# Optimization experiments

Hardware: AMD Instinct MI355X
Metric: run time of the kernel (lower is better)

The kernel has to match this reference:

```python
import jax, jax.numpy as jnp
import numpy as np
from jax import lax

B, W, S, D, H, BH, C = 32, 128, 192, 768, 10, 30, 50
NEG = -1e30  # stand-in for -inf to keep grads NaN-free


def _lstm_dir(x, Wih, Whh, bih, bhh, reverse):
    # x: [B, T, D] -> [B, T, H]; torch gate order i, f, g, o
    xg = jnp.einsum('btd,gd->btg', x, Wih) + bih  # [B, T, 4H]
    if reverse:
        xg = xg[:, ::-1]

    def step(carry, g_t):
        h, c = carry
        g = g_t + h @ Whh.T + bhh
        i, f, gg, o = jnp.split(g, 4, axis=-1)
        c = jax.nn.sigmoid(f) * c + jax.nn.sigmoid(i) * jnp.tanh(gg)
        h = jax.nn.sigmoid(o) * jnp.tanh(c)
        return (h, c), h

    init = (jnp.zeros((x.shape[0], H), x.dtype), jnp.zeros((x.shape[0], H), x.dtype))
    _, hs = lax.scan(step, init, xg.transpose(1, 0, 2))
    hs = hs.transpose(1, 0, 2)
    if reverse:
        hs = hs[:, ::-1]
    return hs


def _biaffine(x, W1, b1, W2, b2, U, bias):
    # DeepBiaffineScorer: MLP+ReLU on each side, bilinear with bias-augmented inputs
    h1 = jax.nn.relu(x @ W1 + b1)
    h2 = jax.nn.relu(x @ W2 + b2)
    ones = jnp.ones(h1.shape[:-1] + (1,), h1.dtype)
    h1a = jnp.concatenate([h1, ones], -1)  # [B, W, BH+1]
    h2a = jnp.concatenate([h2, ones], -1)
    return jnp.einsum('bih,ohg,bjg->bijo', h1a, U, h2a) + bias  # [B, W, W, O]


def _ce_sum(logits, targets, ignore):
    # cross-entropy, reduction='sum', with ignore_index; classes on last axis
    logp = jax.nn.log_softmax(logits, -1)
    valid = targets != ignore
    t = jnp.where(valid, targets, 0)
    picked = jnp.take_along_axis(logp, t[..., None], -1).squeeze(-1)
    return -jnp.sum(jnp.where(valid, picked, 0.0))


def _forward(hiddens, bert2toks, heads, dep_rels, masks,
             Wih_f, Whh_f, bih_f, bhh_f, Wih_b, Whh_b, bih_b, bhh_b,
             un_W1, un_b1, un_W2, un_b2, un_U, un_bias,
             dr_W1, dr_b1, dr_W2, dr_b2, dr_U, dr_bias):
    # mean of the 3 selected BERT layers, then ragged subtoken -> word mean pooling
    means = jnp.mean(hiddens, axis=0)  # [B, S+1, D]
    sub = means[:, 1:]                 # skip [CLS]: [B, S, D]
    seg_sum = jax.vmap(lambda x, s: jax.ops.segment_sum(x, s, num_segments=W))(sub, bert2toks)
    cnt = jax.vmap(lambda s: jax.ops.segment_sum(jnp.ones((S,), sub.dtype), s, num_segments=W))(bert2toks)
    bert_out = seg_sum / jnp.maximum(cnt, 1.0)[..., None]  # [B, W, D]

    # BiLSTM (sent_lens are all full length W, so packing is the identity)
    fwd = _lstm_dir(bert_out, Wih_f, Whh_f, bih_f, bhh_f, False)
    bwd = _lstm_dir(bert_out, Wih_b, Whh_b, bih_b, bhh_b, True)
    unpacked = jnp.concatenate([fwd, bwd], -1)  # [B, W, 2H]

    unlabeled = _biaffine(unpacked, un_W1, un_b1, un_W2, un_b2, un_U, un_bias)[..., 0]  # [B, W, W]
    deprel = _biaffine(unpacked, dr_W1, dr_b1, dr_W2, dr_b2, dr_U, dr_bias)             # [B, W, W, C]

    eye = jnp.eye(W, dtype=bool)
    unlabeled = jnp.where(eye[None], NEG, unlabeled)

    # gather gold-head deprel scores: [B, W, C]
    head_scores = jnp.take_along_axis(deprel, heads[:, :, None, None], axis=2).squeeze(2)
    heads_ = jnp.where(masks, -1, heads)

    deprel_loss = _ce_sum(head_scores, dep_rels, 0)
    depind_loss = _ce_sum(unlabeled[:, 1:], heads_[:, 1:], -1)
    return deprel_loss + depind_loss


def setup_inputs() -> dict:
    key = jax.random.key(0)
    ks = jax.random.split(key, 26)
    hiddens = jax.random.normal(ks[0], (3, B, S + 1, D), jnp.float32)
    # non-decreasing subtoken->word map covering all W words
    bert2toks = jnp.broadcast_to((jnp.arange(S) * W) // S, (B, S)).astype(jnp.int32)
    heads = jax.random.randint(ks[1], (B, W), 0, W)
    heads = jnp.where(heads == jnp.arange(W)[None, :], 0, heads)  # no self-head (diag is -inf)
    dep_rels = jax.random.randint(ks[2], (B, W), 0, C)
    masks = jnp.zeros((B, W), bool)
    sent_lens = jnp.full((B,), W, jnp.int32)
    s = 0.1
    p = lambda k, shape: jax.random.normal(k, shape, jnp.float32) * s
    return dict(
        hiddens=hiddens, bert2toks=bert2toks, heads=heads, dep_rels=dep_rels,
        masks=masks, sent_lens=sent_lens,
        Wih_f=p(ks[3], (4 * H, D)), Whh_f=p(ks[4], (4 * H, H)), bih_f=p(ks[5], (4 * H,)), bhh_f=p(ks[6], (4 * H,)),
        Wih_b=p(ks[7], (4 * H, D)), Whh_b=p(ks[8], (4 * H, H)), bih_b=p(ks[9], (4 * H,)), bhh_b=p(ks[10], (4 * H,)),
        un_W1=p(ks[11], (2 * H, BH)), un_b1=p(ks[12], (BH,)), un_W2=p(ks[13], (2 * H, BH)), un_b2=p(ks[14], (BH,)),
        un_U=p(ks[15], (1, BH + 1, BH + 1)), un_bias=p(ks[16], (1,)),
        dr_W1=p(ks[17], (2 * H, BH)), dr_b1=p(ks[18], (BH,)), dr_W2=p(ks[19], (2 * H, BH)), dr_b2=p(ks[20], (BH,)),
        dr_U=p(ks[21], (C, BH + 1, BH + 1)), dr_bias=p(ks[22], (C,)),
    )


def reference(hiddens, bert2toks, heads, dep_rels, masks, sent_lens,
              Wih_f, Whh_f, bih_f, bhh_f, Wih_b, Whh_b, bih_b, bhh_b,
              un_W1, un_b1, un_W2, un_b2, un_U, un_bias,
              dr_W1, dr_b1, dr_W2, dr_b2, dr_U, dr_bias):
    # sent_lens unused: all sentences are full length, so pack/unpack is identity
    return _forward(hiddens, bert2toks, heads, dep_rels, masks,
                    Wih_f, Whh_f, bih_f, bhh_f, Wih_b, Whh_b, bih_b, bhh_b,
                    un_W1, un_b1, un_W2, un_b2, un_U, un_bias,
                    dr_W1, dr_b1, dr_W2, dr_b2, dr_U, dr_bias)
```

## Files before the change

kernel.cpp:

```cpp
#include <hip/hip_runtime.h>

#define Bn 32
#define Wn 128
#define Sn 192
#define Dn 768
#define Hn 10
#define BHn 30
#define Cn 50
#define NEGV -1e30f

typedef _Float16 h2 __attribute__((ext_vector_type(2)));
typedef _Float16 h8 __attribute__((ext_vector_type(8)));
typedef __fp16 fp16x2 __attribute__((ext_vector_type(2)));
union H8u { h8 v; h2 p[4]; float4 f; };

__device__ __forceinline__ float fsig(float x) {
    return __builtin_amdgcn_rcpf(1.0f + __expf(-x));
}
__device__ __forceinline__ float ftanh(float x) {
    return 1.0f - 2.0f * __builtin_amdgcn_rcpf(1.0f + __expf(2.0f * x));
}
__device__ __forceinline__ float lane_bcast(float v, int srclane) {
    union { float f; int i; } u, w;
    u.f = v;
    w.i = __builtin_amdgcn_readlane(u.i, srclane);
    return w.f;
}
template <int Q>
__device__ __forceinline__ float quad_bcast(float v) {
    union { float f; int i; } u, w;
    u.f = v;
    w.i = __builtin_amdgcn_mov_dpp(u.i, (Q << 6) | (Q << 4) | (Q << 2) | Q, 0xf, 0xf, true);
    return w.f;
}
__device__ __forceinline__ h2 pk16(float a, float b) {
#if __has_builtin(__builtin_amdgcn_cvt_pkrtz)
    union { fp16x2 r; h2 h; } u;
    u.r = __builtin_amdgcn_cvt_pkrtz(a, b);
    return u.h;
#else
    h2 r; r[0] = (_Float16)a; r[1] = (_Float16)b; return r;
#endif
}
__device__ __forceinline__ float dot2f(h2 a, h2 b, float c) {
#if __has_builtin(__builtin_amdgcn_fdot2)
    return __builtin_amdgcn_fdot2(a, b, c, false);
#else
    return c + (float)a[0] * (float)b[0] + (float)a[1] * (float)b[1];
#endif
}

#define XSTR2 52
__global__ __launch_bounds__(256) void k_tokproj(const float* __restrict__ hid,
                                                 const float* __restrict__ Wf,
                                                 const float* __restrict__ Wb,
                                                 float* __restrict__ tokg4,
                                                 float* __restrict__ out) {
    __shared__ h2 xl[64 * XSTR2];
    __shared__ h2 wl[80 * XSTR2];
    int tb = blockIdx.x >> 3;
    int kq = blockIdx.x & 7;
    int b = tb / 3;
    int s0 = (tb % 3) * 64;
    int k0 = kq * 96;
    int tid = threadIdx.x;
    if (blockIdx.x == 0 && tid == 0) out[0] = 0.f;

    for (int idx = tid; idx < 64 * 24; idx += 256) {
        int r = idx / 24, k4 = idx % 24;
        size_t rowbase = ((size_t)b * (Sn + 1) + (s0 + r + 1)) * Dn + k0 + 4 * k4;
        float4 v0 = *(const float4*)(hid + rowbase);
        float4 v1 = *(const float4*)(hid + (size_t)Bn * (Sn + 1) * Dn + rowbase);
        float4 v2 = *(const float4*)(hid + (size_t)2 * Bn * (Sn + 1) * Dn + rowbase);
        h2 a = pk16(v0.x + v1.x + v2.x, v0.y + v1.y + v2.y);
        h2 bb = pk16(v0.z + v1.z + v2.z, v0.w + v1.w + v2.w);
        xl[r * XSTR2 + 2 * k4] = a;
        xl[r * XSTR2 + 2 * k4 + 1] = bb;
    }
    for (int idx = tid; idx < 80 * 24; idx += 256) {
        int co = idx / 24, k4 = idx % 24;
        int dir = co / 40, off = co % 40;
        int j = off >> 2, g = off & 3;
        const float4 w = *(const float4*)((dir ? Wb : Wf) + (g * 10 + j) * Dn + k0 + 4 * k4);
        wl[co * XSTR2 + 2 * k4] = pk16(w.x, w.y);
        wl[co * XSTR2 + 2 * k4 + 1] = pk16(w.z, w.w);
    }
    __syncthreads();

    int tg = tid >> 4;
    int rg = tid & 15;
    float acc[4][5];
#pragma unroll
    for (int tt = 0; tt < 4; ++tt)
#pragma unroll
        for (int rr = 0; rr < 5; ++rr) acc[tt][rr] = 0.f;

    for (int kk = 0; kk < 12; ++kk) {
        H8u xv[4], wv[5];
#pragma unroll
        for (int tt = 0; tt < 4; ++tt)
            xv[tt].v = *(const h8*)(xl + (tg * 4 + tt) * XSTR2 + kk * 4);
#pragma unroll
        for (int rr = 0; rr < 5; ++rr)
            wv[rr].v = *(const h8*)(wl + (rg * 5 + rr) * XSTR2 + kk * 4);
#pragma unroll
        for (int tt = 0; tt < 4; ++tt)
#pragma unroll
            for (int rr = 0; rr < 5; ++rr) {
                float a = acc[tt][rr];
                a = dot2f(xv[tt].p[0], wv[rr].p[0], a);
                a = dot2f(xv[tt].p[1], wv[rr].p[1], a);
                a = dot2f(xv[tt].p[2], wv[rr].p[2], a);
                a = dot2f(xv[tt].p[3], wv[rr].p[3], a);
                acc[tt][rr] = a;
            }
    }
    size_t nbase = (size_t)kq * (Bn * Sn) + (size_t)b * Sn + s0;
#pragma unroll
    for (int tt = 0; tt < 4; ++tt) {
        size_t ob = (nbase + tg * 4 + tt) * 80 + rg * 5;
#pragma unroll
        for (int rr = 0; rr < 5; ++rr) tokg4[ob + rr] = acc[tt][rr];
    }
}

__global__ __launch_bounds__(96) void k_wordmean(const float* __restrict__ tokg4,
                                                 const int* __restrict__ b2t,
                                                 const float* __restrict__ bih_f,
                                                 const float* __restrict__ bih_b,
                                                 float* __restrict__ xg) {
    const size_t NT80 = (size_t)Bn * Sn * 80;
    int bw = blockIdx.x;
    int b = bw >> 7, w = bw & 127;
    int tid = threadIdx.x;
    __shared__ int ws[Sn];
    ws[tid] = b2t[b * Sn + tid];
    ws[96 + tid] = b2t[b * Sn + 96 + tid];
    __syncthreads();
    if (tid >= 80) return;
    int dir = tid / 40, off = tid % 40;
    float acc = 0.f;
    int cnt = 0;
    for (int s = 0; s < Sn; ++s) {
        if (ws[s] == w) {
            ++cnt;
            size_t base = ((size_t)b * Sn + s) * 80 + tid;
#pragma unroll
            for (int p = 0; p < 8; ++p) acc += tokg4[base + p * NT80];
        }
    }
    float inv = 1.0f / (3.0f * (float)(cnt > 0 ? cnt : 1));
    int brow = (off & 3) * 10 + (off >> 2);
    float bias = (dir ? bih_b : bih_f)[brow];
    xg[((size_t)(dir * Bn + b) * Wn + w) * 40 + off] = acc * inv + bias;
}

__global__ __launch_bounds__(64) void k_lstm(const float* __restrict__ xg,
                                             const float* __restrict__ Whh_f, const float* __restrict__ bhh_f,
                                             const float* __restrict__ Whh_b, const float* __restrict__ bhh_b,
                                             float* __restrict__ hs) {
    int lane = threadIdx.x;
    int seq = blockIdx.x;
    int dir = seq >> 5;
    int l = lane < 40 ? lane : 39;
    int j = l >> 2, G = l & 3;

    const float* Whh = dir ? Whh_b : Whh_f;
    const float* bhh = dir ? bhh_b : bhh_f;
    float wk[Hn];
#pragma unroll
    for (int k = 0; k < Hn; ++k) wk[k] = Whh[(G * Hn + j) * Hn + k];
    float bias = bhh[G * Hn + j];

    const float* xbase = xg + (size_t)seq * Wn * 40;
    float* hbase = hs + (size_t)seq * Wn * Hn;
    bool st = (G == 0) && (lane < 40);

    float h = 0.f, c = 0.f;
    int dt = dir ? -1 : 1;
    int t = dir ? (Wn - 1) : 0;
    float xq[8];
#pragma unroll
    for (int q = 0; q < 7; ++q) xq[q] = xbase[(t + q * dt) * 40 + l];

#pragma unroll 8
    for (int step = 0; step < Wn; ++step) {
        float xv = xq[step & 7];
        xq[(step + 7) & 7] = xbase[(t + 7 * dt) * 40 + l];
        float hb[Hn];
#pragma unroll
        for (int k = 0; k < Hn; ++k) hb[k] = lane_bcast(h, 4 * k);
        float ga = xv, gb = bias;
#pragma unroll
        for (int k = 0; k < 5; ++k) ga += wk[k] * hb[k];
#pragma unroll
        for (int k = 5; k < Hn; ++k) gb += wk[k] * hb[k];
        float g = ga + gb;
        float gin = (G == 2) ? 2.f * g : g;
        float s = fsig(gin);
        float av = (G == 2) ? 2.f * s - 1.f : s;
        float ai = quad_bcast<0>(av);
        float af = quad_bcast<1>(av);
        float ag = quad_bcast<2>(av);
        float ao = quad_bcast<3>(av);
        c = af * c + ai * ag;
        h = ao * ftanh(c);
        if (st) hbase[t * Hn + j] = h;
        t += dt;
    }
}

__global__ __launch_bounds__(128) void k_mlp(const float* __restrict__ hs,
                                             const float* __restrict__ uW1, const float* __restrict__ ub1,
                                             const float* __restrict__ uW2, const float* __restrict__ ub2,
                                             const float* __restrict__ dW1, const float* __restrict__ db1,
                                             const float* __restrict__ dW2, const float* __restrict__ db2,
                                             float* __restrict__ hpad) {
    int bt = blockIdx.x;
    int b = bt / Wn, t = bt % Wn;
    __shared__ float x[20];
    int tid = threadIdx.x;
    if (tid < 20) {
        x[tid] = (tid < Hn) ? hs[((size_t)(0 * Bn + b) * Wn + t) * Hn + tid]
                            : hs[((size_t)(1 * Bn + b) * Wn + t) * Hn + (tid - Hn)];
    }
    __syncthreads();
    if (tid >= 124) {
        hpad[((size_t)(tid - 124) * Bn * Wn + bt) * 32 + 31] = 0.f;
        return;
    }
    int which = tid / 31, k = tid % 31;
    float v;
    if (k == 30) {
        v = 1.0f;
    } else {
        const float* Wm;
        const float* bv;
        if (which == 0) { Wm = uW1; bv = ub1; }
        else if (which == 1) { Wm = uW2; bv = ub2; }
        else if (which == 2) { Wm = dW1; bv = db1; }
        else { Wm = dW2; bv = db2; }
        float a = bv[k];
#pragma unroll
        for (int d = 0; d < 20; ++d) a += x[d] * Wm[d * BHn + k];
        v = a > 0.f ? a : 0.f;
    }
    hpad[((size_t)which * Bn * Wn + bt) * 32 + k] = v;
}

__global__ __launch_bounds__(256) void k_drscore(const float* __restrict__ hpad,
                                                 const int* __restrict__ heads,
                                                 const float* __restrict__ U, const float* __restrict__ dbias,
                                                 float* __restrict__ sc) {
    int nc = blockIdx.x & 63;
    int oq = blockIdx.x >> 6;
    __shared__ float Ul[4][992];
    int tid = threadIdx.x;
    for (int idx = tid; idx < 4 * 992; idx += 256) {
        int o = idx / 992, r = idx - o * 992;
        int h = r >> 5, g = r & 31;
        int oo = oq * 4 + o; if (oo >= Cn) oo = Cn - 1;
        Ul[o][r] = (g < 31) ? U[(size_t)oo * 961 + h * 31 + g] : 0.f;
    }
    int w = tid >> 6, lane = tid & 63;
    int o = oq * 4 + w;
    int n = nc * 64 + lane;
    int b = n >> 7;
    int jh = heads[n];
    if (jh < 0 || jh >= Wn) jh = 0;
    const float* h1a = hpad + ((size_t)2 * Bn * Wn + n) * 32;
    const float* h2a = hpad + ((size_t)3 * Bn * Wn + b * Wn + jh) * 32;
    float h2r[32];
    {
        const float4* p = (const float4*)h2a;
#pragma unroll
        for (int q = 0; q < 8; ++q) {
            float4 v = p[q];
            h2r[4 * q + 0] = v.x; h2r[4 * q + 1] = v.y;
            h2r[4 * q + 2] = v.z; h2r[4 * q + 3] = v.w;
        }
    }
    float h1r[32];
    {
        const float4* p = (const float4*)h1a;
#pragma unroll
        for (int q = 0; q < 8; ++q) {
            float4 v = p[q];
            h1r[4 * q + 0] = v.x; h1r[4 * q + 1] = v.y;
            h1r[4 * q + 2] = v.z; h1r[4 * q + 3] = v.w;
        }
    }
    __syncthreads();
    const float* up = Ul[w];
    float acc = 0.f;
    for (int h = 0; h < 31; ++h) {
        float t = 0.f;
#pragma unroll
        for (int g = 0; g < 32; ++g) t += up[h * 32 + g] * h2r[g];
        acc += h1r[h] * t;
    }
    if (o < Cn) sc[(size_t)n * Cn + o] = acc + dbias[o];
}

__global__ __launch_bounds__(256) void k_loss2(const float* __restrict__ hpad,
                                               const float* __restrict__ U0, const float* __restrict__ ubias,
                                               const float* __restrict__ sc,
                                               const int* __restrict__ heads,
                                               const unsigned char* __restrict__ masks,
                                               const int* __restrict__ dep_rels,
                                               float* __restrict__ out) {
    int b = blockIdx.x >> 2;
    int ic = blockIdx.x & 3;
    int tid = threadIdx.x;
    __shared__ float h2s[128 * 36];
    __shared__ float tg[32 * 36];
    __shared__ float U0l[992];
    __shared__ float red[256];
    const float* h1a = hpad + (size_t)b * Wn * 32;
    const float* h2a = hpad + ((size_t)Bn * Wn + b * Wn) * 32;
    for (int idx = tid; idx < 128 * 32; idx += 256)
        h2s[(idx >> 5) * 36 + (idx & 31)] = h2a[idx];
    for (int idx = tid; idx < 992; idx += 256) {
        int g = idx & 31;
        U0l[idx] = (g < 31) ? U0[(idx >> 5) * 31 + g] : 0.f;
    }
    __syncthreads();
    {
        int l = tid & 31, ig = tid >> 5;
        float ur[31];
#pragma unroll
        for (int h = 0; h < 31; ++h) ur[h] = U0l[h * 32 + l];
        for (int ii = 0; ii < 4; ++ii) {
            int il = ig * 4 + ii;
            int i = ic * 32 + il;
            const float4* hp = (const float4*)(h1a + (size_t)i * 32);
            float hr[32];
#pragma unroll
            for (int q = 0; q < 8; ++q) {
                float4 v = hp[q];
                hr[4 * q] = v.x; hr[4 * q + 1] = v.y; hr[4 * q + 2] = v.z; hr[4 * q + 3] = v.w;
            }
            float a = 0.f;
#pragma unroll
            for (int h = 0; h < 31; ++h) a += hr[h] * ur[h];
            tg[il * 36 + l] = a;
        }
    }
    __syncthreads();
    float acc = 0.f;
    {
        int jg = tid & 7, il = tid >> 3;
        int i = ic * 32 + il;
        float ub = ubias[0];
        float4 tq[8];
        const float4* tp = (const float4*)(tg + il * 36);
#pragma unroll
        for (int q = 0; q < 8; ++q) tq[q] = tp[q];
        float m = -3e38f, lsum = 0.f, sh = 0.f;
        int hd = heads[b * Wn + i];
        for (int jj = 0; jj < 16; ++jj) {
            int j = jg * 16 + ((jj + jg) & 15);
            const float4* h2p = (const float4*)(h2s + j * 36);
            float s = ub;
#pragma unroll
            for (int q = 0; q < 8; ++q) {
                float4 hq = h2p[q];
                s += tq[q].x * hq.x + tq[q].y * hq.y + tq[q].z * hq.z + tq[q].w * hq.w;
            }
            if (j == i) s = NEGV;
            float mn = fmaxf(m, s);
            lsum = lsum * __expf(m - mn) + __expf(s - mn);
            m = mn;
            if (j == hd) sh = s;
        }
        float shv = (jg == (hd >> 4)) ? sh : 0.f;
        float mm = m, ll = lsum;
#pragma unroll
        for (int off = 1; off < 8; off <<= 1) {
            float m2 = __shfl_xor(mm, off);
            float l2 = __shfl_xor(ll, off);
            float mn = fmaxf(mm, m2);
            ll = ll * __expf(mm - mn) + l2 * __expf(m2 - mn);
            mm = mn;
            shv += __shfl_xor(shv, off);
        }
        if (jg == 0 && i >= 1 && !masks[b * Wn + i])
            acc += -(shv - (mm + __logf(ll)));
    }
    if (tid < 32) {
        int n = b * Wn + ic * 32 + tid;
        int r = dep_rels[n];
        if (r != 0 && r < Cn) {
            const float* sp = sc + (size_t)n * Cn;
            float mm = sp[0];
            for (int o = 1; o < Cn; ++o) mm = fmaxf(mm, sp[o]);
            float e = 0.f;
            for (int o = 0; o < Cn; ++o) e += __expf(sp[o] - mm);
            acc += -(sp[r] - (mm + __logf(e)));
        }
    }
    red[tid] = acc;
    __syncthreads();
    for (int off = 128; off > 0; off >>= 1) {
        if (tid < off) red[tid] += red[tid + off];
        __syncthreads();
    }
    if (tid == 0) atomicAdd(out, red[0]);
}

extern "C" void kernel_launch(void* const* d_in, const int* in_sizes, int n_in,
                              void* d_out, int out_size, void* d_ws, size_t ws_size,
                              hipStream_t stream) {
    const float* hiddens = (const float*)d_in[0];
    const int* b2t = (const int*)d_in[1];
    const int* heads = (const int*)d_in[2];
    const int* dep_rels = (const int*)d_in[3];
    const unsigned char* masks = (const unsigned char*)d_in[4];
    const float* Wih_f = (const float*)d_in[6];
    const float* Whh_f = (const float*)d_in[7];
    const float* bih_f = (const float*)d_in[8];
    const float* bhh_f = (const float*)d_in[9];
    const float* Wih_b = (const float*)d_in[10];
    const float* Whh_b = (const float*)d_in[11];
    const float* bih_b = (const float*)d_in[12];
    const float* bhh_b = (const float*)d_in[13];
    const float* un_W1 = (const float*)d_in[14];
    const float* un_b1 = (const float*)d_in[15];
    const float* un_W2 = (const float*)d_in[16];
    const float* un_b2 = (const float*)d_in[17];
    const float* un_U  = (const float*)d_in[18];
    const float* un_bias = (const float*)d_in[19];
    const float* dr_W1 = (const float*)d_in[20];
    const float* dr_b1 = (const float*)d_in[21];
    const float* dr_W2 = (const float*)d_in[22];
    const float* dr_b2 = (const float*)d_in[23];
    const float* dr_U  = (const float*)d_in[24];
    const float* dr_bias = (const float*)d_in[25];

    char* p = (char*)d_ws;
    float* tokg4 = (float*)p;     p += (size_t)8 * Bn * Sn * 80 * 4;
    float* xg = (float*)p;        p += (size_t)2 * Bn * Wn * 40 * 4;
    float* hs = (float*)p;        p += (size_t)2 * Bn * Wn * Hn * 4;
    float* hpad = (float*)p;      p += (size_t)4 * Bn * Wn * 32 * 4;
    float* sc = (float*)p;        p += (size_t)Bn * Wn * Cn * 4;

    float* out = (float*)d_out;

    k_tokproj<<<96 * 8, 256, 0, stream>>>(hiddens, Wih_f, Wih_b, tokg4, out);
    k_wordmean<<<Bn * Wn, 96, 0, stream>>>(tokg4, b2t, bih_f, bih_b, xg);
    k_lstm<<<64, 64, 0, stream>>>(xg, Whh_f, bhh_f, Whh_b, bhh_b, hs);
    k_mlp<<<Bn * Wn, 128, 0, stream>>>(hs, un_W1, un_b1, un_W2, un_b2,
                                       dr_W1, dr_b1, dr_W2, dr_b2, hpad);
    k_drscore<<<13 * 64, 256, 0, stream>>>(hpad, heads, dr_U, dr_bias, sc);
    k_loss2<<<Bn * 4, 256, 0, stream>>>(hpad, un_U, un_bias, sc, heads, masks, dep_rels, out);
}
```

Measured before the change: 94.72 us.

## Cut token-projection split-K from 8 to 2 with register-prefetched weight chunks

The token projection kernel now splits the 768-wide reduction into 2 halves instead of 8. Each block loads a 384-wide slice of activations into LDS and walks four weight chunks, prefetching the next chunk into registers while computing the current one. This shrinks the partial-sum buffer by 4x and reduces the word-mean kernel's per-token reads from 8 partials to 2. The cost is only 192 blocks instead of 768, which lowers parallelism, plus more LDS per block and more weight registers, which may reduce occupancy.

Result: slower. 97.05 us (+2.5%).

```diff
diff --git a/kernel.cpp b/kernel.cpp
--- a/kernel.cpp
+++ b/kernel.cpp
@@ -50,40 +50,51 @@
 #endif
 }
 
-#define XSTR2 52
+#define XST 196
+#define WST 52
 __global__ __launch_bounds__(256) void k_tokproj(const float* __restrict__ hid,
                                                  const float* __restrict__ Wf,
                                                  const float* __restrict__ Wb,
-                                                 float* __restrict__ tokg4,
+                                                 float* __restrict__ tokg2,
                                                  float* __restrict__ out) {
-    __shared__ h2 xl[64 * XSTR2];
-    __shared__ h2 wl[80 * XSTR2];
-    int tb = blockIdx.x >> 3;
-    int kq = blockIdx.x & 7;
+    __shared__ h2 xl[64 * XST];
+    __shared__ h2 wl[80 * WST];
+    int tb = blockIdx.x >> 1;
+    int kh = blockIdx.x & 1;
     int b = tb / 3;
     int s0 = (tb % 3) * 64;
-    int k0 = kq * 96;
+    int k0 = kh * 384;
     int tid = threadIdx.x;
     if (blockIdx.x == 0 && tid == 0) out[0] = 0.f;
 
-    for (int idx = tid; idx < 64 * 24; idx += 256) {
-        int r = idx / 24, k4 = idx % 24;
+    float4 wreg[8];
+#define W_ISSUE(kc_) { _Pragma("unroll") \
+    for (int it = 0; it < 8; ++it) { \
+        int idx = tid + it * 256; int ii = idx < 1920 ? idx : 0; \
+        int co = ii / 24, k4 = ii % 24; \
+        int dir = co / 40, off = co % 40; \
+        int jj = off >> 2, gg = off & 3; \
+        wreg[it] = *(const float4*)((dir ? Wb : Wf) + (gg * 10 + jj) * Dn + k0 + (kc_) * 96 + 4 * k4); \
+    } }
+#define W_WRITE() { _Pragma("unroll") \
+    for (int it = 0; it < 8; ++it) { \
+        int idx = tid + it * 256; \
+        if (idx < 1920) { \
+            int co = idx / 24, k4 = idx % 24; \
+            wl[co * WST + 2 * k4] = pk16(wreg[it].x, wreg[it].y); \
+            wl[co * WST + 2 * k4 + 1] = pk16(wreg[it].z, wreg[it].w); \
+        } \
+    } }
+
+    W_ISSUE(0);
+    for (int idx = tid; idx < 64 * 96; idx += 256) {
+        int r = idx / 96, k4 = idx % 96;
         size_t rowbase = ((size_t)b * (Sn + 1) + (s0 + r + 1)) * Dn + k0 + 4 * k4;
         float4 v0 = *(const float4*)(hid + rowbase);
         float4 v1 = *(const float4*)(hid + (size_t)Bn * (Sn + 1) * Dn + rowbase);
         float4 v2 = *(const float4*)(hid + (size_t)2 * Bn * (Sn + 1) * Dn + rowbase);
-        h2 a = pk16(v0.x + v1.x + v2.x, v0.y + v1.y + v2.y);
-        h2 bb = pk16(v0.z + v1.z + v2.z, v0.w + v1.w + v2.w);
-        xl[r * XSTR2 + 2 * k4] = a;
-        xl[r * XSTR2 + 2 * k4 + 1] = bb;
-    }
-    for (int idx = tid; idx < 80 * 24; idx += 256) {
-        int co = idx / 24, k4 = idx % 24;
-        int dir = co / 40, off = co % 40;
-        int j = off >> 2, g = off & 3;
-        const float4 w = *(const float4*)((dir ? Wb : Wf) + (g * 10 + j) * Dn + k0 + 4 * k4);
-        wl[co * XSTR2 + 2 * k4] = pk16(w.x, w.y);
-        wl[co * XSTR2 + 2 * k4 + 1] = pk16(w.z, w.w);
+        xl[r * XST + 2 * k4] = pk16(v0.x + v1.x + v2.x, v0.y + v1.y + v2.y);
+        xl[r * XST + 2 * k4 + 1] = pk16(v0.z + v1.z + v2.z, v0.w + v1.w + v2.w);
     }
     __syncthreads();
 
@@ -95,36 +106,45 @@
 #pragma unroll
         for (int rr = 0; rr < 5; ++rr) acc[tt][rr] = 0.f;
 
-    for (int kk = 0; kk < 12; ++kk) {
-        H8u xv[4], wv[5];
-#pragma unroll
-        for (int tt = 0; tt < 4; ++tt)
-            xv[tt].v = *(const h8*)(xl + (tg * 4 + tt) * XSTR2 + kk * 4);
-#pragma unroll
-        for (int rr = 0; rr < 5; ++rr)
-            wv[rr].v = *(const h8*)(wl + (rg * 5 + rr) * XSTR2 + kk * 4);
-#pragma unroll
-        for (int tt = 0; tt < 4; ++tt)
-#pragma unroll
-            for (int rr = 0; rr < 5; ++rr) {
-                float a = acc[tt][rr];
-                a = dot2f(xv[tt].p[0], wv[rr].p[0], a);
-                a = dot2f(xv[tt].p[1], wv[rr].p[1], a);
-                a = dot2f(xv[tt].p[2], wv[rr].p[2], a);
-                a = dot2f(xv[tt].p[3], wv[rr].p[3], a);
-                acc[tt][rr] = a;
-            }
-    }
-    size_t nbase = (size_t)kq * (Bn * Sn) + (size_t)b * Sn + s0;
+    for (int kc = 0; kc < 4; ++kc) {
+        W_WRITE();
+        __syncthreads();
+        if (kc < 3) W_ISSUE(kc + 1);
+#pragma unroll 2
+        for (int kk = 0; kk < 12; ++kk) {
+            H8u xv[4], wv[5];
+#pragma unroll
+            for (int tt = 0; tt < 4; ++tt)
+                xv[tt].v = *(const h8*)(xl + (tg * 4 + tt) * XST + kc * 48 + kk * 4);
+#pragma unroll
+            for (int rr = 0; rr < 5; ++rr)
+                wv[rr].v = *(const h8*)(wl + (rg * 5 + rr) * WST + kk * 4);
+#pragma unroll
+            for (int tt = 0; tt < 4; ++tt)
+#pragma unroll
+                for (int rr = 0; rr < 5; ++rr) {
+                    float a = acc[tt][rr];
+                    a = dot2f(xv[tt].p[0], wv[rr].p[0], a);
+                    a = dot2f(xv[tt].p[1], wv[rr].p[1], a);
+                    a = dot2f(xv[tt].p[2], wv[rr].p[2], a);
+                    a = dot2f(xv[tt].p[3], wv[rr].p[3], a);
+                    acc[tt][rr] = a;
+                }
+        }
+        __syncthreads();
+    }
+    size_t nbase = (size_t)kh * (Bn * Sn) + (size_t)b * Sn + s0;
 #pragma unroll
     for (int tt = 0; tt < 4; ++tt) {
         size_t ob = (nbase + tg * 4 + tt) * 80 + rg * 5;
 #pragma unroll
-        for (int rr = 0; rr < 5; ++rr) tokg4[ob + rr] = acc[tt][rr];
-    }
-}
-
-__global__ __launch_bounds__(96) void k_wordmean(const float* __restrict__ tokg4,
+        for (int rr = 0; rr < 5; ++rr) tokg2[ob + rr] = acc[tt][rr];
+    }
+#undef W_ISSUE
+#undef W_WRITE
+}
+
+__global__ __launch_bounds__(96) void k_wordmean(const float* __restrict__ tokg2,
                                                  const int* __restrict__ b2t,
                                                  const float* __restrict__ bih_f,
                                                  const float* __restrict__ bih_b,
@@ -145,8 +165,7 @@
         if (ws[s] == w) {
             ++cnt;
             size_t base = ((size_t)b * Sn + s) * 80 + tid;
-#pragma unroll
-            for (int p = 0; p < 8; ++p) acc += tokg4[base + p * NT80];
+            acc += tokg2[base] + tokg2[base + NT80];
         }
     }
     float inv = 1.0f / (3.0f * (float)(cnt > 0 ? cnt : 1));
@@ -438,7 +457,7 @@
     const float* dr_bias = (const float*)d_in[25];
 
     char* p = (char*)d_ws;
-    float* tokg4 = (float*)p;     p += (size_t)8 * Bn * Sn * 80 * 4;
+    float* tokg2 = (float*)p;     p += (size_t)2 * Bn * Sn * 80 * 4;
     float* xg = (float*)p;        p += (size_t)2 * Bn * Wn * 40 * 4;
     float* hs = (float*)p;        p += (size_t)2 * Bn * Wn * Hn * 4;
     float* hpad = (float*)p;      p += (size_t)4 * Bn * Wn * 32 * 4;
@@ -446,8 +465,8 @@
 
     float* out = (float*)d_out;
 
-    k_tokproj<<<96 * 8, 256, 0, stream>>>(hiddens, Wih_f, Wih_b, tokg4, out);
-    k_wordmean<<<Bn * Wn, 96, 0, stream>>>(tokg4, b2t, bih_f, bih_b, xg);
+    k_tokproj<<<96 * 2, 256, 0, stream>>>(hiddens, Wih_f, Wih_b, tokg2, out);
+    k_wordmean<<<Bn * Wn, 96, 0, stream>>>(tokg2, b2t, bih_f, bih_b, xg);
     k_lstm<<<64, 64, 0, stream>>>(xg, Whh_f, bhh_f, Whh_b, bhh_b, hs);
     k_mlp<<<Bn * Wn, 128, 0, stream>>>(hs, un_W1, un_b1, un_W2, un_b2,
                                        dr_W1, dr_b1, dr_W2, dr_b2, hpad);
```
